# Kernel optimization log

Measured on AMD Instinct MI355X. Metric: run time of the kernel, lower is better.

Reference implementation:

```python
import jax, jax.numpy as jnp
import numpy as np

CURV = 0.9            # geoopt PoincareBall(0.9)
SQRT_C = CURV ** 0.5
MIN_NORM = 1e-15
PROJ_EPS = 4e-3       # geoopt float32 boundary eps
ATANH_EPS = 1e-7
COS_EPS = 1e-8        # torch.cosine_similarity eps


def _norm(x):
    return jnp.sqrt(jnp.maximum(jnp.sum(x * x, axis=-1, keepdims=True), MIN_NORM * MIN_NORM))


def _project(x):
    # project onto ball of radius (1-eps)/sqrt(c)
    n = jnp.maximum(_norm(x), MIN_NORM)
    maxnorm = (1.0 - PROJ_EPS) / SQRT_C
    return jnp.where(n > maxnorm, x / n * maxnorm, x)


def expmap0(u):
    n = jnp.maximum(_norm(u), MIN_NORM)
    gamma = jnp.tanh(SQRT_C * n) * u / (SQRT_C * n)
    return _project(gamma)


def mobius_add(x, y):
    c = CURV
    x2 = jnp.sum(x * x, axis=-1, keepdims=True)
    y2 = jnp.sum(y * y, axis=-1, keepdims=True)
    xy = jnp.sum(x * y, axis=-1, keepdims=True)
    num = (1.0 + 2.0 * c * xy + c * y2) * x + (1.0 - c * x2) * y
    den = 1.0 + 2.0 * c * xy + c * c * x2 * y2
    return num / jnp.maximum(den, MIN_NORM)


def pdist(x, y):
    # dist(x,y) = 2/sqrt(c) * artanh(sqrt(c) * ||(-x) (+) y||)
    d = mobius_add(-x, y)
    n = _norm(d)[..., 0]
    z = jnp.clip(SQRT_C * n, -1.0 + ATANH_EPS, 1.0 - ATANH_EPS)
    return 2.0 / SQRT_C * jnp.arctanh(z)


def cos_sim(a, b):
    na = jnp.maximum(jnp.sqrt(jnp.sum(a * a, axis=-1)), COS_EPS)
    nb = jnp.maximum(jnp.sqrt(jnp.sum(b * b, axis=-1)), COS_EPS)
    return jnp.sum(a * b, axis=-1) / (na * nb)


def setup_inputs() -> dict:
    key = jax.random.key(0)
    ks = jax.random.split(key, 11)
    B, L, Ls, C, Lc, H, R = 4, 512, 128, 20, 128, 768, 512
    s = 0.02  # keep projected embeddings in a realistic range
    return {
        "text_out": jax.random.normal(ks[0], (B, L, H), jnp.float32),
        "summary_out": jax.random.normal(ks[1], (B, Ls, H), jnp.float32),
        "candidate_out": jax.random.normal(ks[2], (B, C, Lc, H), jnp.float32),
        "W_d": jax.random.normal(ks[3], (H, R), jnp.float32) * s,
        "W_s": jax.random.normal(ks[4], (H, R), jnp.float32) * s,
        "W_c": jax.random.normal(ks[5], (H, R), jnp.float32) * s,
        "W_p": jax.random.normal(ks[6], (R, R), jnp.float32) * s,
        "conv_w1": jax.random.normal(ks[7], (1, H, R), jnp.float32) * s,
        "conv_b1": jax.random.normal(ks[8], (R,), jnp.float32) * s,
        "conv_w2": jax.random.normal(ks[9], (2, H, R), jnp.float32) * s,
        "conv_b2": jax.random.normal(ks[10], (R,), jnp.float32) * s,
    }


def _forward(text_out, summary_out, candidate_out, W_d, W_s, W_c, W_p,
             conv_w1, conv_b1, conv_w2, conv_b2):
    # --- document ---
    doc_emb = expmap0(text_out[:, 0, :] @ W_d)                       # [B,R]

    # NGramers (max_gram=2, eval mode so dropout is identity)
    x = text_out[:, 1:-1, :]                                         # [B,L-2,H]
    y1 = jax.nn.relu(jnp.einsum('blh,hr->blr', x, conv_w1[0]) + conv_b1)
    y2 = jax.nn.relu(jnp.einsum('blh,hr->blr', x[:, :-1], conv_w2[0])
                     + jnp.einsum('blh,hr->blr', x[:, 1:], conv_w2[1]) + conv_b2)
    gram = jnp.concatenate([y1, y2], axis=1)                         # [B,2L-5,R]

    doc_word_emb = expmap0(jnp.einsum('blr,rk->blk', gram, W_p))     # [B,T,R]
    doc_inter = 1.0 / pdist(doc_word_emb, doc_emb[:, None, :])       # [B,T]

    # --- summary ---
    summary_emb = expmap0(jnp.max(summary_out, axis=1) @ W_s)        # [B,R]
    summary_score = -pdist(summary_emb, doc_emb) ** 2                # [B]
    sum_inter = 1.0 / pdist(doc_word_emb, summary_emb[:, None, :])   # [B,T]
    summary_score = summary_score + cos_sim(doc_inter, sum_inter)    # [B]

    # --- candidates ---
    cand_emb = expmap0(jnp.einsum('bch,hr->bcr', jnp.max(candidate_out, axis=2), W_c))  # [B,C,R]
    score = -pdist(cand_emb, doc_emb[:, None, :]) ** 2               # [B,C]
    cand_inter = 1.0 / pdist(doc_word_emb[:, None, :, :], cand_emb[:, :, None, :])      # [B,C,T]
    score = score + cos_sim(doc_inter[:, None, :], cand_inter)       # [B,C]
    return score, summary_score


def reference(text_out, summary_out, candidate_out, W_d, W_s, W_c, W_p,
              conv_w1, conv_b1, conv_w2, conv_b2):
    return _forward(text_out, summary_out, candidate_out, W_d, W_s, W_c, W_p,
                    conv_w1, conv_b1, conv_w2, conv_b2)
```

## Files before the change

kernel.cpp:

```cpp
#include <hip/hip_runtime.h>
#include <math.h>

#define SQRTC  0.94868329805051381f
#define MAXN   (0.996f/SQRTC)
#define OME_CLIP (1.0f - 0.996f*0.996f)
#define TWO_OVER_SQRTC 2.1081851067789197f

typedef unsigned short u16;
typedef __attribute__((ext_vector_type(8))) short bf8;
typedef __attribute__((ext_vector_type(4))) float f4;

__device__ __forceinline__ u16 f2bf(float f){
    union { float f; unsigned int i; } v; v.f = f;
    unsigned int x = v.i;
    unsigned int lsb = (x >> 16) & 1u;
    x += 0x7fffu + lsb;
    return (u16)(x >> 16);
}
__device__ __forceinline__ float bf2f(u16 u){
    union { unsigned int i; float f; } v; v.i = ((unsigned int)u) << 16; return v.f;
}

__device__ __forceinline__ float pdist_stable(float ome_x, float ome_y, float t){
    float u = 1.0f - ome_x, v = 1.0f - ome_y;
    float den = fmaxf(1.0f - 1.8f*t + u*v, 1e-15f);
    float q = ome_x*ome_y/den;
    q = fminf(fmaxf(q, 2.0e-7f), 1.0f);
    float z = sqrtf(fmaxf(1.0f - q, 0.0f));
    float at = 0.5f * logf((1.0f+z)*(1.0f+z)/q);
    return TWO_OVER_SQRTC * at;
}

__device__ __forceinline__ void expmap_scale_ome(float sum, float* fout, float* omeout){
    float nraw = sqrtf(fmaxf(sum, 1e-30f));
    float n = fmaxf(nraw, 1e-15f);
    float sn = SQRTC*n;
    float th = tanhf(sn);
    float factor = th/sn;
    float gn = factor*nraw;
    if (gn > MAXN){ *fout = factor*(MAXN/gn); *omeout = OME_CLIP; }
    else { *fout = factor; *omeout = fmaxf((1.0f-th)*(1.0f+th), 1e-12f); }
}

__global__ __launch_bounds__(256)
void k_stage1(const float* __restrict__ summ, const float* __restrict__ cand,
              const float* __restrict__ text,
              const float* __restrict__ w1, const float* __restrict__ w2,
              const float* __restrict__ wp,
              float* __restrict__ smax, float* __restrict__ cmax,
              u16* __restrict__ textb, u16* __restrict__ w1t,
              u16* __restrict__ w2t, u16* __restrict__ wpt)
{
    __shared__ float shm[1056];
    int bx = blockIdx.x;
    int t = threadIdx.x;
    if (bx < 1008){
        int row = bx / 12, ht = bx - row*12;
        int lane = t & 63, lg = t >> 6;
        int h = ht*64 + lane;
        const float* in = (row < 4) ? (summ + (long long)row*128*768)
                                    : (cand + (long long)(row-4)*128*768);
        const float* p = in + (long long)(lg*32)*768 + h;
        float m = -INFINITY;
        #pragma unroll 8
        for (int l = 0; l < 32; l++) m = fmaxf(m, p[l*768]);
        shm[t] = m; __syncthreads();
        if (t < 64){
            float mm = fmaxf(fmaxf(shm[t], shm[t+64]), fmaxf(shm[t+128], shm[t+192]));
            if (row < 4) smax[row*768 + h] = mm;
            else cmax[(row-4)*768 + h] = mm;
        }
        return;
    }
    int pb = bx - 1008;
    if (pb < 768){
        int base = pb*2048 + t*8;
        float4 a = *(const float4*)(text + base);
        float4 b = *(const float4*)(text + base + 4);
        *(ushort4*)(textb + base)     = make_ushort4(f2bf(a.x), f2bf(a.y), f2bf(a.z), f2bf(a.w));
        *(ushort4*)(textb + base + 4) = make_ushort4(f2bf(b.x), f2bf(b.y), f2bf(b.z), f2bf(b.w));
        return;
    }
    int j = pb - 768;
    const float* in; u16* outp; int K;
    if (j < 384){ in = w1; outp = w1t; K = 768; }
    else if (j < 1152){ j -= 384; in = w2; outp = w2t; K = 1536; }
    else { j -= 1152; in = wp; outp = wpt; K = 512; }
    const int N = 512, ntile = N/32;
    int k0 = (j/ntile)*32, n0 = (j - (j/ntile)*ntile)*32;
    int tx = t & 31, ty = t >> 5;
    #pragma unroll
    for (int i = 0; i < 4; i++)
        shm[(ty*4+i)*33 + tx] = in[(long long)(k0 + ty*4 + i)*N + n0 + tx];
    __syncthreads();
    #pragma unroll
    for (int i = 0; i < 4; i++)
        outp[(long long)(n0 + ty*4 + i)*K + k0 + tx] = f2bf(shm[tx*33 + ty*4+i]);
}

__global__ __launch_bounds__(256)
void k_stage2(const u16* __restrict__ textb,
              const u16* __restrict__ w1t, const u16* __restrict__ w2t,
              const float* __restrict__ cb1, const float* __restrict__ cb2,
              const float* __restrict__ text,
              const float* __restrict__ smax, const float* __restrict__ cmax,
              const float* __restrict__ W_d, const float* __restrict__ W_s,
              const float* __restrict__ W_c,
              u16* __restrict__ gram, float* __restrict__ emb_all)
{
    __shared__ char smem[8192];
    int bx = blockIdx.x;
    int t = threadIdx.x;
    if (bx < 512){
        u16 (*As)[32] = (u16(*)[32])smem;
        u16 (*Bs)[32] = (u16(*)[32])(smem + 4096);
        int xx = bx & 63, yy = bx >> 6;
        int job = xx & 1;
        int m0 = (xx >> 1) * 64;
        int n0 = yy * 64;
        int K   = job ? 1536 : 768;
        int M   = job ? 2036 : 2040;
        int rpb = job ? 509 : 510;
        int ob  = job ? 510 : 0;
        const u16* Bt = job ? w2t : w1t;
        const float* bias = job ? cb2 : cb1;
        int sr = t >> 2, sk = (t & 3) << 3;
        const u16* Arow = nullptr;
        { int gm = m0 + sr; if (gm < M){ int b = gm/rpb, l = gm - b*rpb;
            Arow = textb + (long long)b*393216 + (long long)(l+1)*768; } }
        const u16* Brow = Bt + (long long)(n0 + sr)*K;
        int lane = t & 63, wv = t >> 6;
        int fm = lane & 15, fq = lane >> 4;
        int arow = wv*16 + fm;
        f4 acc0 = {0,0,0,0}, acc1 = {0,0,0,0}, acc2 = {0,0,0,0}, acc3 = {0,0,0,0};
        for (int k0 = 0; k0 < K; k0 += 32){
            bf8 av = {};
            if (Arow) av = *(const bf8*)(Arow + k0 + sk);
            bf8 bv = *(const bf8*)(Brow + k0 + sk);
            *(bf8*)&As[sr][sk] = av;
            *(bf8*)&Bs[sr][sk] = bv;
            __syncthreads();
            bf8 af = *(const bf8*)&As[arow][fq*8];
            bf8 b0 = *(const bf8*)&Bs[ 0+fm][fq*8];
            bf8 b1 = *(const bf8*)&Bs[16+fm][fq*8];
            bf8 b2 = *(const bf8*)&Bs[32+fm][fq*8];
            bf8 b3 = *(const bf8*)&Bs[48+fm][fq*8];
            acc0 = __builtin_amdgcn_mfma_f32_16x16x32_bf16(af, b0, acc0, 0, 0, 0);
            acc1 = __builtin_amdgcn_mfma_f32_16x16x32_bf16(af, b1, acc1, 0, 0, 0);
            acc2 = __builtin_amdgcn_mfma_f32_16x16x32_bf16(af, b2, acc2, 0, 0, 0);
            acc3 = __builtin_amdgcn_mfma_f32_16x16x32_bf16(af, b3, acc3, 0, 0, 0);
            __syncthreads();
        }
        int col = n0 + fm;
        float bv0 = bias[col], bv1 = bias[col+16], bv2 = bias[col+32], bv3 = bias[col+48];
        #pragma unroll
        for (int i = 0; i < 4; i++){
            int row = m0 + wv*16 + fq*4 + i;
            if (row >= M) continue;
            int b = row/rpb, l = row - b*rpb;
            long long orow = (long long)b*1019 + ob + l;
            u16* gp = gram + orow*512;
            gp[col]      = f2bf(fmaxf(acc0[i] + bv0, 0.f));
            gp[col + 16] = f2bf(fmaxf(acc1[i] + bv1, 0.f));
            gp[col + 32] = f2bf(fmaxf(acc2[i] + bv2, 0.f));
            gp[col + 48] = f2bf(fmaxf(acc3[i] + bv3, 0.f));
        }
        return;
    }
    {
        int eb = bx - 512;
        int row = eb >> 3, nt = eb & 7;
        float* a   = (float*)smem;
        float* red = (float*)smem + 768;
        const float* A; const float* W;
        if (row < 4){ A = text + (long long)row*512*768; W = W_d; }
        else if (row < 8){ A = smax + (long long)(row-4)*768; W = W_s; }
        else { A = cmax + (long long)(row-8)*768; W = W_c; }
        for (int k = t; k < 768; k += 256) a[k] = A[k];
        __syncthreads();
        int lane = t & 63, kg = t >> 6;
        int col = nt*64 + lane;
        const float* Wp = W + (long long)(kg*192)*512 + col;
        float acc = 0.f;
        #pragma unroll 8
        for (int k = 0; k < 192; k++) acc += a[kg*192 + k] * Wp[k*512];
        red[t] = acc; __syncthreads();
        if (t < 64) emb_all[(long long)row*512 + col] = red[t] + red[t+64] + red[t+128] + red[t+192];
    }
}

__global__ __launch_bounds__(256)
void k_stage3(const u16* __restrict__ gram, const u16* __restrict__ wpt,
              u16* __restrict__ dwe_b,
              float* __restrict__ emb_all, float* __restrict__ ome_all,
              u16* __restrict__ emb_b)
{
    __shared__ char smem[8192];
    int bx = blockIdx.x;
    int t = threadIdx.x;
    if (bx < 512){
        u16 (*As)[32] = (u16(*)[32])smem;
        u16 (*Bs)[32] = (u16(*)[32])(smem + 4096);
        const int K = 512, M = 4076;
        int m0 = (bx >> 3) * 64;
        int n0 = (bx & 7) * 64;
        int sr = t >> 2, sk = (t & 3) << 3;
        const u16* Arow = (m0 + sr < M) ? (gram + (long long)(m0 + sr)*512) : nullptr;
        const u16* Brow = wpt + (long long)(n0 + sr)*K;
        int lane = t & 63, wv = t >> 6;
        int fm = lane & 15, fq = lane >> 4;
        int arow = wv*16 + fm;
        f4 acc0 = {0,0,0,0}, acc1 = {0,0,0,0}, acc2 = {0,0,0,0}, acc3 = {0,0,0,0};
        for (int k0 = 0; k0 < K; k0 += 32){
            bf8 av = {};
            if (Arow) av = *(const bf8*)(Arow + k0 + sk);
            bf8 bv = *(const bf8*)(Brow + k0 + sk);
            *(bf8*)&As[sr][sk] = av;
            *(bf8*)&Bs[sr][sk] = bv;
            __syncthreads();
            bf8 af = *(const bf8*)&As[arow][fq*8];
            bf8 b0 = *(const bf8*)&Bs[ 0+fm][fq*8];
            bf8 b1 = *(const bf8*)&Bs[16+fm][fq*8];
            bf8 b2 = *(const bf8*)&Bs[32+fm][fq*8];
            bf8 b3 = *(const bf8*)&Bs[48+fm][fq*8];
            acc0 = __builtin_amdgcn_mfma_f32_16x16x32_bf16(af, b0, acc0, 0, 0, 0);
            acc1 = __builtin_amdgcn_mfma_f32_16x16x32_bf16(af, b1, acc1, 0, 0, 0);
            acc2 = __builtin_amdgcn_mfma_f32_16x16x32_bf16(af, b2, acc2, 0, 0, 0);
            acc3 = __builtin_amdgcn_mfma_f32_16x16x32_bf16(af, b3, acc3, 0, 0, 0);
            __syncthreads();
        }
        int col = n0 + fm;
        #pragma unroll
        for (int i = 0; i < 4; i++){
            int row = m0 + wv*16 + fq*4 + i;
            if (row >= M) continue;
            u16* dp = dwe_b + (long long)row*512;
            dp[col]      = f2bf(acc0[i]);
            dp[col + 16] = f2bf(acc1[i]);
            dp[col + 32] = f2bf(acc2[i]);
            dp[col + 48] = f2bf(acc3[i]);
        }
        return;
    }
    {
        float* red = (float*)smem;
        int row = bx - 512;
        float* X = emb_all + (long long)row*512;
        float2 u = *(float2*)(X + t*2);
        red[t] = u.x*u.x + u.y*u.y; __syncthreads();
        for (int s = 128; s > 0; s >>= 1){ if (t < s) red[t] += red[t+s]; __syncthreads(); }
        float f, ome;
        expmap_scale_ome(red[0], &f, &ome);
        float sx = u.x*f, sy = u.y*f;
        *(float2*)(X + t*2) = make_float2(sx, sy);
        u16* Xb = emb_b + (long long)row*512;
        Xb[t*2]   = f2bf(sx);
        Xb[t*2+1] = f2bf(sy);
        if (t == 0) ome_all[row] = ome;
    }
}

__global__ __launch_bounds__(256)
void k_dots_mfma(const u16* __restrict__ dwe_b, const u16* __restrict__ emb_b,
                 const float* __restrict__ ome_all,
                 float* __restrict__ doc_inter, float* __restrict__ sum_inter,
                 float* __restrict__ cand_inter)
{
    __shared__ u16 As[64][32];
    __shared__ u16 Bs[32][32];
    __shared__ float ssp[64][4];
    __shared__ float ssl[64];
    __shared__ float oyl[22];
    int bx = blockIdx.x;
    int b  = bx >> 4;
    int m0 = (bx & 15) * 64;
    int t = threadIdx.x;
    int sra = t >> 2, ska = (t & 3) << 3;
    const u16* Arow = (m0 + sra < 1019) ? (dwe_b + (long long)(b*1019 + m0 + sra)*512) : nullptr;
    const u16* Brow = nullptr;
    if (t < 128){
        int n = t >> 2;
        if (n < 22){
            int ei = (n == 0) ? b : (n == 1) ? 4 + b : 8 + b*20 + (n - 2);
            Brow = emb_b + (long long)ei*512;
        }
    }
    if (t < 22) oyl[t] = ome_all[(t == 0) ? b : (t == 1) ? 4 + b : 8 + b*20 + (t - 2)];
    int lane = t & 63, wv = t >> 6;
    int fm = lane & 15, fq = lane >> 4;
    f4 acc0 = {0,0,0,0}, acc1 = {0,0,0,0};
    float ssq = 0.f;
    for (int k0 = 0; k0 < 512; k0 += 32){
        bf8 av = {};
        if (Arow) av = *(const bf8*)(Arow + k0 + ska);
        *(bf8*)&As[sra][ska] = av;
        if (t < 128){
            bf8 bv = {};
            if (Brow) bv = *(const bf8*)(Brow + k0 + ((t & 3) << 3));
            *(bf8*)&Bs[t >> 2][(t & 3) << 3] = bv;
        }
        #pragma unroll
        for (int j = 0; j < 8; j++){ float x = bf2f(((u16*)&av)[j]); ssq += x*x; }
        __syncthreads();
        bf8 af = *(const bf8*)&As[wv*16 + fm][fq*8];
        bf8 b0 = *(const bf8*)&Bs[fm][fq*8];
        bf8 b1 = *(const bf8*)&Bs[16 + fm][fq*8];
        acc0 = __builtin_amdgcn_mfma_f32_16x16x32_bf16(af, b0, acc0, 0, 0, 0);
        acc1 = __builtin_amdgcn_mfma_f32_16x16x32_bf16(af, b1, acc1, 0, 0, 0);
        __syncthreads();
    }
    ssp[sra][t & 3] = ssq; __syncthreads();
    if (t < 64) ssl[t] = ssp[t][0] + ssp[t][1] + ssp[t][2] + ssp[t][3];
    __syncthreads();
    #pragma unroll
    for (int i = 0; i < 4; i++){
        int rtile = wv*16 + fq*4 + i;
        int row = m0 + rtile;
        if (row >= 1019) continue;
        float f, ox;
        expmap_scale_ome(ssl[rtile], &f, &ox);
        long long grow = (long long)b*1019 + row;
        #pragma unroll
        for (int g = 0; g < 2; g++){
            int c = g*16 + fm;
            if (c >= 22) continue;
            float s = (g ? acc1[i] : acc0[i]) * f;
            float dist = pdist_stable(ox, oyl[c], s);
            float inv = 1.0f/fmaxf(dist, 1e-12f);
            if (c == 0) doc_inter[grow] = inv;
            else if (c == 1) sum_inter[grow] = inv;
            else cand_inter[((long long)(b*20 + (c - 2)))*1019 + row] = inv;
        }
    }
}

__global__ __launch_bounds__(256)
void k_final(const float* __restrict__ doc_inter, const float* __restrict__ sum_inter,
             const float* __restrict__ cand_inter,
             const float* __restrict__ emb_all, const float* __restrict__ ome_all,
             float* __restrict__ out)
{
    __shared__ float r0[256], r1[256], r2[256], r3[256];
    int j = blockIdx.x, t = threadIdx.x;
    int b; const float *a, *bb; int xi, yi; int outIdx;
    if (j < 80){
        b = j/20;
        a  = doc_inter + b*1019;
        bb = cand_inter + (long long)j*1019;
        xi = 8 + j; yi = b;
        outIdx = j;
    } else {
        b = j - 80;
        a  = doc_inter + b*1019;
        bb = sum_inter + b*1019;
        xi = 4 + b; yi = b;
        outIdx = 80 + b;
    }
    const float* xe = emb_all + (long long)xi*512;
    const float* ye = emb_all + (long long)yi*512;
    float ox = ome_all[xi], oy = ome_all[yi];
    float saa = 0.f, sbb = 0.f, sab = 0.f, st = 0.f;
    for (int l = t; l < 1019; l += 256){ float av = a[l], bv = bb[l]; saa += av*av; sbb += bv*bv; sab += av*bv; }
    for (int k = t; k < 512; k += 256) st += xe[k]*ye[k];
    r0[t] = saa; r1[t] = sbb; r2[t] = sab; r3[t] = st; __syncthreads();
    for (int s = 128; s > 0; s >>= 1){
        if (t < s){ r0[t] += r0[t+s]; r1[t] += r1[t+s]; r2[t] += r2[t+s]; r3[t] += r3[t+s]; }
        __syncthreads();
    }
    if (t == 0){
        float na = fmaxf(sqrtf(r0[0]), 1e-8f);
        float nb = fmaxf(sqrtf(r1[0]), 1e-8f);
        float cosv = r2[0] / (na*nb);
        float pd = pdist_stable(ox, oy, r3[0]);
        out[outIdx] = -pd*pd + cosv;
    }
}

extern "C" void kernel_launch(void* const* d_in, const int* in_sizes, int n_in,
                              void* d_out, int out_size, void* d_ws, size_t ws_size,
                              hipStream_t stream) {
    const float* text = (const float*)d_in[0];
    const float* summ = (const float*)d_in[1];
    const float* cand = (const float*)d_in[2];
    const float* W_d  = (const float*)d_in[3];
    const float* W_s  = (const float*)d_in[4];
    const float* W_c  = (const float*)d_in[5];
    const float* W_p  = (const float*)d_in[6];
    const float* cw1  = (const float*)d_in[7];
    const float* cb1  = (const float*)d_in[8];
    const float* cw2  = (const float*)d_in[9];
    const float* cb2  = (const float*)d_in[10];
    float* out = (float*)d_out;

    const int B = 4, C = 20, H = 768;

    char* base = (char*)d_ws;
    size_t off = 0;
    auto allocF = [&](size_t n)->float*{ float* p = (float*)(base + off); off += ((n*4) + 255) & ~(size_t)255; return p; };
    auto allocU = [&](size_t n)->u16*{ u16* p = (u16*)(base + off); off += ((n*2) + 255) & ~(size_t)255; return p; };

    float* smax = allocF(B*H);
    float* cmax = allocF(B*C*H);
    float* emb_all = allocF(88*512);
    float* ome_all = allocF(88);
    u16* emb_b = allocU(88*512);
    u16* textb = allocU(4*512*768);
    u16* w1t   = allocU(512*768);
    u16* w2t   = allocU(512*1536);
    u16* wpt   = allocU(512*512);
    u16* gram  = allocU(4076*512);
    u16* dwe_b = allocU(4076*512);
    float* doc_inter = allocF(4076);
    float* sum_inter = allocF(4076);
    float* cand_inter= allocF(B*C*1019);

    k_stage1<<<3184, 256, 0, stream>>>(summ, cand, text, cw1, cw2, W_p,
                                       smax, cmax, textb, w1t, w2t, wpt);

    k_stage2<<<1216, 256, 0, stream>>>(textb, w1t, w2t, cb1, cb2,
                                       text, smax, cmax, W_d, W_s, W_c,
                                       gram, emb_all);

    k_stage3<<<600, 256, 0, stream>>>(gram, wpt, dwe_b, emb_all, ome_all, emb_b);

    k_dots_mfma<<<64, 256, 0, stream>>>(dwe_b, emb_b, ome_all,
                                        doc_inter, sum_inter, cand_inter);

    k_final<<<84, 256, 0, stream>>>(doc_inter, sum_inter, cand_inter,
                                    emb_all, ome_all, out);
}
```

Baseline: 162.7 us.

## Use direct global-to-LDS loads with XOR swizzle and K=64 tiles in GEMMs

The two MFMA GEMM paths in stage2 and stage3 now load tiles with global_load_lds, which writes global memory straight into LDS without going through registers. The K step doubles to 64, halving the number of barrier pairs per tile, and an XOR swizzle on the LDS columns is meant to avoid bank conflicts on the fragment reads. Out-of-range rows are clamped to the last valid row instead of being zero-filled, which relies on the epilogue skipping those rows. LDS use per block doubles to 16 KB, and there is still no double buffering, so load latency stays exposed before each barrier.

```diff
diff --git a/kernel.cpp b/kernel.cpp
--- a/kernel.cpp
+++ b/kernel.cpp
@@ -19,6 +19,13 @@
 }
 __device__ __forceinline__ float bf2f(u16 u){
     union { unsigned int i; float f; } v; v.i = ((unsigned int)u) << 16; return v.f;
+}
+
+__device__ __forceinline__ void gload16(void* lds, const void* g){
+    __builtin_amdgcn_global_load_lds(
+        (const __attribute__((address_space(1))) unsigned int*)g,
+        (__attribute__((address_space(3))) unsigned int*)lds,
+        16, 0, 0);
 }
 
 __device__ __forceinline__ float pdist_stable(float ome_x, float ome_y, float t){
@@ -108,12 +115,12 @@
               const float* __restrict__ W_c,
               u16* __restrict__ gram, float* __restrict__ emb_all)
 {
-    __shared__ char smem[8192];
+    __shared__ char smem[16384];
     int bx = blockIdx.x;
     int t = threadIdx.x;
     if (bx < 512){
-        u16 (*As)[32] = (u16(*)[32])smem;
-        u16 (*Bs)[32] = (u16(*)[32])(smem + 4096);
+        u16* As = (u16*)smem;
+        u16* Bs = (u16*)(smem + 8192);
         int xx = bx & 63, yy = bx >> 6;
         int job = xx & 1;
         int m0 = (xx >> 1) * 64;
@@ -124,31 +131,57 @@
         int ob  = job ? 510 : 0;
         const u16* Bt = job ? w2t : w1t;
         const float* bias = job ? cb2 : cb1;
-        int sr = t >> 2, sk = (t & 3) << 3;
-        const u16* Arow = nullptr;
-        { int gm = m0 + sr; if (gm < M){ int b = gm/rpb, l = gm - b*rpb;
-            Arow = textb + (long long)b*393216 + (long long)(l+1)*768; } }
-        const u16* Brow = Bt + (long long)(n0 + sr)*K;
+
+        int r0 = t >> 3;
+        int co = (((t & 7) ^ (r0 & 7)) << 3);
+
+        int gm0 = m0 + r0;      if (gm0 >= M) gm0 = M - 1;
+        int gm1 = m0 + r0 + 32; if (gm1 >= M) gm1 = M - 1;
+        int ab0 = gm0 / rpb, al0 = gm0 - ab0*rpb;
+        int ab1 = gm1 / rpb, al1 = gm1 - ab1*rpb;
+        const u16* a0 = textb + (long long)ab0*393216 + (long long)(al0+1)*768 + co;
+        const u16* a1 = textb + (long long)ab1*393216 + (long long)(al1+1)*768 + co;
+        const u16* bp0 = Bt + (long long)(n0 + r0)*K      + co;
+        const u16* bp1 = Bt + (long long)(n0 + r0 + 32)*K + co;
+        u16* lA0 = As + t*8;
+        u16* lA1 = As + (256 + t)*8;
+        u16* lB0 = Bs + t*8;
+        u16* lB1 = Bs + (256 + t)*8;
+
         int lane = t & 63, wv = t >> 6;
         int fm = lane & 15, fq = lane >> 4;
         int arow = wv*16 + fm;
+        int aswz = arow & 7, bswz = fm & 7;
+        int aoff0 = arow*64 + ((fq     ^ aswz) << 3);
+        int aoff1 = arow*64 + (((4+fq) ^ aswz) << 3);
+        int boff0 = ((fq     ^ bswz) << 3);
+        int boff1 = (((4+fq) ^ bswz) << 3);
+
         f4 acc0 = {0,0,0,0}, acc1 = {0,0,0,0}, acc2 = {0,0,0,0}, acc3 = {0,0,0,0};
-        for (int k0 = 0; k0 < K; k0 += 32){
-            bf8 av = {};
-            if (Arow) av = *(const bf8*)(Arow + k0 + sk);
-            bf8 bv = *(const bf8*)(Brow + k0 + sk);
-            *(bf8*)&As[sr][sk] = av;
-            *(bf8*)&Bs[sr][sk] = bv;
+        for (int k0 = 0; k0 < K; k0 += 64){
+            gload16(lA0, a0 + k0);
+            gload16(lA1, a1 + k0);
+            gload16(lB0, bp0 + k0);
+            gload16(lB1, bp1 + k0);
             __syncthreads();
-            bf8 af = *(const bf8*)&As[arow][fq*8];
-            bf8 b0 = *(const bf8*)&Bs[ 0+fm][fq*8];
-            bf8 b1 = *(const bf8*)&Bs[16+fm][fq*8];
-            bf8 b2 = *(const bf8*)&Bs[32+fm][fq*8];
-            bf8 b3 = *(const bf8*)&Bs[48+fm][fq*8];
-            acc0 = __builtin_amdgcn_mfma_f32_16x16x32_bf16(af, b0, acc0, 0, 0, 0);
-            acc1 = __builtin_amdgcn_mfma_f32_16x16x32_bf16(af, b1, acc1, 0, 0, 0);
-            acc2 = __builtin_amdgcn_mfma_f32_16x16x32_bf16(af, b2, acc2, 0, 0, 0);
-            acc3 = __builtin_amdgcn_mfma_f32_16x16x32_bf16(af, b3, acc3, 0, 0, 0);
+            bf8 af0 = *(const bf8*)(As + aoff0);
+            bf8 af1 = *(const bf8*)(As + aoff1);
+            bf8 b00 = *(const bf8*)(Bs + (fm   )*64 + boff0);
+            bf8 b10 = *(const bf8*)(Bs + (16+fm)*64 + boff0);
+            bf8 b20 = *(const bf8*)(Bs + (32+fm)*64 + boff0);
+            bf8 b30 = *(const bf8*)(Bs + (48+fm)*64 + boff0);
+            bf8 b01 = *(const bf8*)(Bs + (fm   )*64 + boff1);
+            bf8 b11 = *(const bf8*)(Bs + (16+fm)*64 + boff1);
+            bf8 b21 = *(const bf8*)(Bs + (32+fm)*64 + boff1);
+            bf8 b31 = *(const bf8*)(Bs + (48+fm)*64 + boff1);
+            acc0 = __builtin_amdgcn_mfma_f32_16x16x32_bf16(af0, b00, acc0, 0, 0, 0);
+            acc1 = __builtin_amdgcn_mfma_f32_16x16x32_bf16(af0, b10, acc1, 0, 0, 0);
+            acc2 = __builtin_amdgcn_mfma_f32_16x16x32_bf16(af0, b20, acc2, 0, 0, 0);
+            acc3 = __builtin_amdgcn_mfma_f32_16x16x32_bf16(af0, b30, acc3, 0, 0, 0);
+            acc0 = __builtin_amdgcn_mfma_f32_16x16x32_bf16(af1, b01, acc0, 0, 0, 0);
+            acc1 = __builtin_amdgcn_mfma_f32_16x16x32_bf16(af1, b11, acc1, 0, 0, 0);
+            acc2 = __builtin_amdgcn_mfma_f32_16x16x32_bf16(af1, b21, acc2, 0, 0, 0);
+            acc3 = __builtin_amdgcn_mfma_f32_16x16x32_bf16(af1, b31, acc3, 0, 0, 0);
             __syncthreads();
         }
         int col = n0 + fm;
@@ -195,38 +228,63 @@
               float* __restrict__ emb_all, float* __restrict__ ome_all,
               u16* __restrict__ emb_b)
 {
-    __shared__ char smem[8192];
+    __shared__ char smem[16384];
     int bx = blockIdx.x;
     int t = threadIdx.x;
     if (bx < 512){
-        u16 (*As)[32] = (u16(*)[32])smem;
-        u16 (*Bs)[32] = (u16(*)[32])(smem + 4096);
+        u16* As = (u16*)smem;
+        u16* Bs = (u16*)(smem + 8192);
         const int K = 512, M = 4076;
         int m0 = (bx >> 3) * 64;
         int n0 = (bx & 7) * 64;
-        int sr = t >> 2, sk = (t & 3) << 3;
-        const u16* Arow = (m0 + sr < M) ? (gram + (long long)(m0 + sr)*512) : nullptr;
-        const u16* Brow = wpt + (long long)(n0 + sr)*K;
+
+        int r0 = t >> 3;
+        int co = (((t & 7) ^ (r0 & 7)) << 3);
+        int gm0 = m0 + r0;      if (gm0 >= M) gm0 = M - 1;
+        int gm1 = m0 + r0 + 32; if (gm1 >= M) gm1 = M - 1;
+        const u16* a0 = gram + (long long)gm0*512 + co;
+        const u16* a1 = gram + (long long)gm1*512 + co;
+        const u16* bp0 = wpt + (long long)(n0 + r0)*K      + co;
+        const u16* bp1 = wpt + (long long)(n0 + r0 + 32)*K + co;
+        u16* lA0 = As + t*8;
+        u16* lA1 = As + (256 + t)*8;
+        u16* lB0 = Bs + t*8;
+        u16* lB1 = Bs + (256 + t)*8;
+
         int lane = t & 63, wv = t >> 6;
         int fm = lane & 15, fq = lane >> 4;
         int arow = wv*16 + fm;
+        int aswz = arow & 7, bswz = fm & 7;
+        int aoff0 = arow*64 + ((fq     ^ aswz) << 3);
+        int aoff1 = arow*64 + (((4+fq) ^ aswz) << 3);
+        int boff0 = ((fq     ^ bswz) << 3);
+        int boff1 = (((4+fq) ^ bswz) << 3);
+
         f4 acc0 = {0,0,0,0}, acc1 = {0,0,0,0}, acc2 = {0,0,0,0}, acc3 = {0,0,0,0};
-        for (int k0 = 0; k0 < K; k0 += 32){
-            bf8 av = {};
-            if (Arow) av = *(const bf8*)(Arow + k0 + sk);
-            bf8 bv = *(const bf8*)(Brow + k0 + sk);
-            *(bf8*)&As[sr][sk] = av;
-            *(bf8*)&Bs[sr][sk] = bv;
+        for (int k0 = 0; k0 < K; k0 += 64){
+            gload16(lA0, a0 + k0);
+            gload16(lA1, a1 + k0);
+            gload16(lB0, bp0 + k0);
+            gload16(lB1, bp1 + k0);
             __syncthreads();
-            bf8 af = *(const bf8*)&As[arow][fq*8];
-            bf8 b0 = *(const bf8*)&Bs[ 0+fm][fq*8];
-            bf8 b1 = *(const bf8*)&Bs[16+fm][fq*8];
-            bf8 b2 = *(const bf8*)&Bs[32+fm][fq*8];
-            bf8 b3 = *(const bf8*)&Bs[48+fm][fq*8];
-            acc0 = __builtin_amdgcn_mfma_f32_16x16x32_bf16(af, b0, acc0, 0, 0, 0);
-            acc1 = __builtin_amdgcn_mfma_f32_16x16x32_bf16(af, b1, acc1, 0, 0, 0);
-            acc2 = __builtin_amdgcn_mfma_f32_16x16x32_bf16(af, b2, acc2, 0, 0, 0);
-            acc3 = __builtin_amdgcn_mfma_f32_16x16x32_bf16(af, b3, acc3, 0, 0, 0);
+            bf8 af0 = *(const bf8*)(As + aoff0);
+            bf8 af1 = *(const bf8*)(As + aoff1);
+            bf8 b00 = *(const bf8*)(Bs + (fm   )*64 + boff0);
+            bf8 b10 = *(const bf8*)(Bs + (16+fm)*64 + boff0);
+            bf8 b20 = *(const bf8*)(Bs + (32+fm)*64 + boff0);
+            bf8 b30 = *(const bf8*)(Bs + (48+fm)*64 + boff0);
+            bf8 b01 = *(const bf8*)(Bs + (fm   )*64 + boff1);
+            bf8 b11 = *(const bf8*)(Bs + (16+fm)*64 + boff1);
+            bf8 b21 = *(const bf8*)(Bs + (32+fm)*64 + boff1);
+            bf8 b31 = *(const bf8*)(Bs + (48+fm)*64 + boff1);
+            acc0 = __builtin_amdgcn_mfma_f32_16x16x32_bf16(af0, b00, acc0, 0, 0, 0);
+            acc1 = __builtin_amdgcn_mfma_f32_16x16x32_bf16(af0, b10, acc1, 0, 0, 0);
+            acc2 = __builtin_amdgcn_mfma_f32_16x16x32_bf16(af0, b20, acc2, 0, 0, 0);
+            acc3 = __builtin_amdgcn_mfma_f32_16x16x32_bf16(af0, b30, acc3, 0, 0, 0);
+            acc0 = __builtin_amdgcn_mfma_f32_16x16x32_bf16(af1, b01, acc0, 0, 0, 0);
+            acc1 = __builtin_amdgcn_mfma_f32_16x16x32_bf16(af1, b11, acc1, 0, 0, 0);
+            acc2 = __builtin_amdgcn_mfma_f32_16x16x32_bf16(af1, b21, acc2, 0, 0, 0);
+            acc3 = __builtin_amdgcn_mfma_f32_16x16x32_bf16(af1, b31, acc3, 0, 0, 0);
             __syncthreads();
         }
         int col = n0 + fm;
```

Result: faster. 150.5 us (-7.5%).
